# Kernel tuning notes

Hardware: AMD Instinct MI355X
Metric: run time of the kernel (lower is better)

The kernel has to match this reference:

```python
import jax, jax.numpy as jnp
import numpy as np

IN, OUT, RANK, ALPHA, GS = 4096, 4096, 16, 32, 64
SCALING = ALPHA / RANK  # alpha / rank = 2.0


def setup_inputs() -> dict:
    key = jax.random.key(0)
    k1, k2, k3, k4, k5 = jax.random.split(key, 5)
    x = jax.random.normal(k1, (4, 2048, IN), dtype=jnp.float32)
    # signed int4 codes in [-8, 7]
    q_w = jax.random.randint(k2, (OUT, IN), -8, 8, dtype=jnp.int32)
    # per-group absmax scales (positive, small)
    scales = jax.random.uniform(k3, (OUT, IN // GS), dtype=jnp.float32) * 0.02 + 1e-3
    lora_A = jax.random.normal(k4, (RANK, IN), dtype=jnp.float32) * 0.02
    lora_B = jax.random.normal(k5, (OUT, RANK), dtype=jnp.float32) * 0.02
    return {"x": x, "q_w": q_w, "scales": scales, "lora_A": lora_A, "lora_B": lora_B}


def reference(x, q_w, scales, lora_A, lora_B):
    # Dequantize 4-bit base weight: blockwise symmetric, group_size=GS along in_features.
    # W[o, g*GS + j] = q[o, g*GS + j] * scales[o, g]
    W = (q_w.astype(jnp.float32).reshape(OUT, IN // GS, GS)
         * scales[:, :, None]).reshape(OUT, IN)
    # Frozen base layer: y = x @ W^T (Linear4bit, no bias)
    base_output = jnp.einsum('bsi,oi->bso', x, W)
    # LoRA branch (dropout p=0 -> identity): B(A(x)) * (alpha/rank)
    lora_output = jnp.einsum('bsr,or->bso', jnp.einsum('bsi,ri->bsr', x, lora_A), lora_B) * SCALING
    return base_output + lora_output
```

## Files before the change

kernel.cpp:

```cpp
#include <hip/hip_runtime.h>
#include <hip/hip_bf16.h>


typedef unsigned short u16;
typedef __attribute__((ext_vector_type(8))) short bf16x8;
typedef __attribute__((ext_vector_type(4))) float f32x4;
typedef __attribute__((ext_vector_type(4))) int i32x4;

#define M_DIM 8192
#define N_DIM 4096
#define K_DIM 4096
#define BK 64
#define KT_MAIN 64
#define NT 65

__device__ static inline u16 f2bf(float f) {
    union { float f; unsigned u; } v; v.f = f;
    unsigned r = v.u + 0x7fffu + ((v.u >> 16) & 1u);
    return (u16)(r >> 16);
}

__device__ static inline void gload16(const void* g, void* s) {
    __builtin_amdgcn_global_load_lds(
        (const __attribute__((address_space(1))) void*)g,
        (__attribute__((address_space(3))) void*)s, 16, 0, 0);
}

__global__ __launch_bounds__(256) void wprep_kernel(
        const int* __restrict__ q, const float* __restrict__ scales,
        u16* __restrict__ Wb) {
    int idx = blockIdx.x * 256 + threadIdx.x;
    int o  = idx >> 9;
    int kc = (idx & 511) << 3;
    float s = scales[(o << 6) + (kc >> 6)];
    const i32x4* qp = (const i32x4*)(q + (size_t)o * K_DIM + kc);
    i32x4 q0 = __builtin_nontemporal_load(qp);
    i32x4 q1 = __builtin_nontemporal_load(qp + 1);
    ushort4 r0, r1;
    r0.x = f2bf((float)q0.x * s); r0.y = f2bf((float)q0.y * s);
    r0.z = f2bf((float)q0.z * s); r0.w = f2bf((float)q0.w * s);
    r1.x = f2bf((float)q1.x * s); r1.y = f2bf((float)q1.y * s);
    r1.z = f2bf((float)q1.z * s); r1.w = f2bf((float)q1.w * s);
    *(ushort4*)&Wb[(size_t)o * K_DIM + kc]     = r0;
    *(ushort4*)&Wb[(size_t)o * K_DIM + kc + 4] = r1;
}

__global__ __launch_bounds__(256) void bprep_kernel(
        const float* __restrict__ lora_B, u16* __restrict__ B2) {
    int idx = blockIdx.x * 256 + threadIdx.x;
    int o = idx >> 6, r = idx & 63;
    B2[idx] = (r < 16) ? f2bf(lora_B[o * 16 + r]) : (u16)0;
}

__global__ __launch_bounds__(256) void xprep_kernel(
        const float* __restrict__ x, const float* __restrict__ lora_A,
        u16* __restrict__ xb, u16* __restrict__ t2) {
    const int tid = threadIdx.x, w = tid >> 6, l = tid & 63;
    const int rb = blockIdx.x * 8 + w * 2;
    float acc[2][16];
#pragma unroll
    for (int j = 0; j < 2; ++j)
#pragma unroll
        for (int r = 0; r < 16; ++r) acc[j][r] = 0.f;

    for (int i = 0; i < 16; ++i) {
        int k0 = i * 256 + l * 4;
        f32x4 x0 = __builtin_nontemporal_load(
                        (const f32x4*)&x[(size_t)rb * K_DIM + k0]);
        f32x4 x1 = __builtin_nontemporal_load(
                        (const f32x4*)&x[(size_t)(rb + 1) * K_DIM + k0]);
        ushort4 o0, o1;
        o0.x = f2bf(x0.x); o0.y = f2bf(x0.y); o0.z = f2bf(x0.z); o0.w = f2bf(x0.w);
        o1.x = f2bf(x1.x); o1.y = f2bf(x1.y); o1.z = f2bf(x1.z); o1.w = f2bf(x1.w);
        *(ushort4*)&xb[(size_t)rb * K_DIM + k0]       = o0;
        *(ushort4*)&xb[(size_t)(rb + 1) * K_DIM + k0] = o1;
#pragma unroll
        for (int r = 0; r < 16; ++r) {
            f32x4 av = *(const f32x4*)&lora_A[(size_t)r * K_DIM + k0];
            acc[0][r] += x0.x * av.x + x0.y * av.y + x0.z * av.z + x0.w * av.w;
            acc[1][r] += x1.x * av.x + x1.y * av.y + x1.z * av.z + x1.w * av.w;
        }
    }
#pragma unroll
    for (int j = 0; j < 2; ++j)
#pragma unroll
        for (int r = 0; r < 16; ++r) {
            float v = acc[j][r];
            v += __shfl_xor(v, 32); v += __shfl_xor(v, 16);
            v += __shfl_xor(v, 8);  v += __shfl_xor(v, 4);
            v += __shfl_xor(v, 2);  v += __shfl_xor(v, 1);
            acc[j][r] = v;
        }
    float lo = 0.f, hi = 0.f;
#pragma unroll
    for (int j = 0; j < 2; ++j)
#pragma unroll
        for (int c = 0; c < 8; ++c)
            if (l == j * 32 + c) { lo = acc[j][2 * c]; hi = acc[j][2 * c + 1]; }
    unsigned pack = (unsigned)f2bf(2.0f * lo) | ((unsigned)f2bf(2.0f * hi) << 16);
    *(unsigned*)&t2[(size_t)(rb + (l >> 5)) * 64 + (l & 31) * 2] = pack;
}

__global__ __launch_bounds__(512, 2) void qlora_gemm(
        const u16* __restrict__ xb, const u16* __restrict__ Wb,
        const u16* __restrict__ t2, const u16* __restrict__ B2,
        float* __restrict__ out) {
    __shared__ u16 lds[2][32768];
    int bid = blockIdx.x;
    int x8 = bid & 7, sq = bid >> 3;
    int bm = (x8 & 1) * 16 + (sq & 15);
    int bn = (x8 >> 1) * 4 + (sq >> 4);
    const int tid = threadIdx.x, w = tid >> 6, l = tid & 63;
    const int wr = w >> 2, wc = w & 3;
    const int fr = l & 15, fq = l >> 4;
    const int s0 = fq ^ (fr & 7);

    const int sw16 = ((l & 7) ^ ((l >> 3) & 7)) << 4;
    const int rl   = w * 8 + (l >> 3);
    const int rA0  = bm * 256 + rl;
    const int rB0  = bn * 256 + rl;
    char* ldsC = (char*)&lds[0][0];
    const int dst = w * 1024 + l * 16;

    const int arow = (wr * 128 + fr) * 128;
    const int brow = 32768 + (wc * 64 + fr) * 128;

    f32x4 acc[8][4] = {};

    auto stage = [&](int kt, int buf) {
        char* base = ldsC + buf * 65536;
        if (kt < KT_MAIN) {
            size_t ko = (size_t)kt * 128;
#pragma unroll
            for (int o = 0; o < 4; ++o) {
                gload16((const char*)xb + ((size_t)(rA0 + o * 64) * 8192 + sw16) + ko,
                        base + dst + o * 8192);
                gload16((const char*)Wb + ((size_t)(rB0 + o * 64) * 8192 + sw16) + ko,
                        base + 32768 + dst + o * 8192);
            }
        } else {
#pragma unroll
            for (int o = 0; o < 4; ++o) {
                gload16((const char*)t2 + ((size_t)(rA0 + o * 64) * 128 + sw16),
                        base + dst + o * 8192);
                gload16((const char*)B2 + ((size_t)(rB0 + o * 64) * 128 + sw16),
                        base + 32768 + dst + o * 8192);
            }
        }
    };

    stage(0, 0);
    asm volatile("s_waitcnt vmcnt(0)" ::: "memory");
    __builtin_amdgcn_s_barrier();
    asm volatile("" ::: "memory");

    bf16x8 a0[8], b0[4], a1[8], b1[4];
#pragma unroll
    for (int j = 0; j < 4; ++j)
        b0[j] = *(const bf16x8*)(ldsC + brow + j * 2048 + s0 * 16);
#pragma unroll
    for (int i = 0; i < 8; ++i)
        a0[i] = *(const bf16x8*)(ldsC + arow + i * 2048 + s0 * 16);

    for (int t = 0; t < NT; ++t) {
        const char* cb = ldsC + (t & 1) * 65536;

#pragma unroll
        for (int j = 0; j < 4; ++j)
            b1[j] = *(const bf16x8*)(cb + brow + j * 2048 + (s0 ^ 4) * 16);
#pragma unroll
        for (int i = 0; i < 8; ++i)
            a1[i] = *(const bf16x8*)(cb + arow + i * 2048 + (s0 ^ 4) * 16);
        if (t + 1 < NT) stage(t + 1, (t + 1) & 1);
        __builtin_amdgcn_sched_barrier(0);

        __builtin_amdgcn_s_setprio(1);
#pragma unroll
        for (int i = 0; i < 8; ++i)
#pragma unroll
            for (int j = 0; j < 4; ++j)
                acc[i][j] = __builtin_amdgcn_mfma_f32_16x16x32_bf16(
                                a0[i], b0[j], acc[i][j], 0, 0, 0);
        __builtin_amdgcn_s_setprio(0);
        __builtin_amdgcn_sched_barrier(0);

        asm volatile("s_waitcnt lgkmcnt(0)" ::: "memory");
        asm volatile("s_waitcnt vmcnt(0)" ::: "memory");
        __builtin_amdgcn_s_barrier();
        asm volatile("" ::: "memory");

        if (t + 1 < NT) {
            const char* nb = ldsC + ((t + 1) & 1) * 65536;
#pragma unroll
            for (int j = 0; j < 4; ++j)
                b0[j] = *(const bf16x8*)(nb + brow + j * 2048 + s0 * 16);
#pragma unroll
            for (int i = 0; i < 8; ++i)
                a0[i] = *(const bf16x8*)(nb + arow + i * 2048 + s0 * 16);
        }
        __builtin_amdgcn_sched_barrier(0);

        __builtin_amdgcn_s_setprio(1);
#pragma unroll
        for (int i = 0; i < 8; ++i)
#pragma unroll
            for (int j = 0; j < 4; ++j)
                acc[i][j] = __builtin_amdgcn_mfma_f32_16x16x32_bf16(
                                a1[i], b1[j], acc[i][j], 0, 0, 0);
        __builtin_amdgcn_s_setprio(0);
        __builtin_amdgcn_sched_barrier(0);
    }

    float* obase = out + (size_t)(bm * 256 + wr * 128 + fq * 4) * N_DIM
                       + bn * 256 + wc * 64 + fr;
#pragma unroll
    for (int i = 0; i < 8; ++i)
#pragma unroll
        for (int j = 0; j < 4; ++j)
#pragma unroll
            for (int r = 0; r < 4; ++r)
                obase[(size_t)(i * 16 + r) * N_DIM + j * 16] = acc[i][j][r];
}

extern "C" void kernel_launch(void* const* d_in, const int* in_sizes, int n_in,
                              void* d_out, int out_size, void* d_ws, size_t ws_size,
                              hipStream_t stream) {
    const float* x      = (const float*)d_in[0];
    const int*   qw     = (const int*)d_in[1];
    const float* scales = (const float*)d_in[2];
    const float* lora_A = (const float*)d_in[3];
    const float* lora_B = (const float*)d_in[4];
    float* out = (float*)d_out;

    char* ws = (char*)d_ws;
    u16* xb = (u16*)(ws);
    u16* Wb = (u16*)(ws + 67108864);
    u16* t2 = (u16*)(ws + 100663296);
    u16* B2 = (u16*)(ws + 101711872);

    wprep_kernel<<<8192, 256, 0, stream>>>(qw, scales, Wb);
    bprep_kernel<<<1024, 256, 0, stream>>>(lora_B, B2);
    xprep_kernel<<<1024, 256, 0, stream>>>(x, lora_A, xb, t2);
    qlora_gemm<<<dim3(512), 512, 0, stream>>>(xb, Wb, t2, B2, out);
}
```

Before: 314.1 us.

## Merge prep kernels into one launch and deepen GEMM prefetch pipeline

Folds the three preprocessing kernels (weight dequant, LoRA-B pad, x conversion plus LoRA-A projection) into one kernel dispatched by block index. This removes two launches and lets the three jobs run concurrently on the GPU. The GEMM main loop is restructured to issue the global-to-LDS stage for the next tile at the top of each iteration, with a two-stage prologue. LDS fragment reads are interleaved with the MFMA half-steps so reads of one half overlap compute on the other, at the cost of more complex waitcnt ordering in the double-buffered LDS.

```diff
diff --git a/kernel.cpp b/kernel.cpp
--- a/kernel.cpp
+++ b/kernel.cpp
@@ -26,79 +26,79 @@
         (__attribute__((address_space(3))) void*)s, 16, 0, 0);
 }
 
-__global__ __launch_bounds__(256) void wprep_kernel(
+__global__ __launch_bounds__(256) void prep_kernel(
         const int* __restrict__ q, const float* __restrict__ scales,
-        u16* __restrict__ Wb) {
-    int idx = blockIdx.x * 256 + threadIdx.x;
-    int o  = idx >> 9;
-    int kc = (idx & 511) << 3;
-    float s = scales[(o << 6) + (kc >> 6)];
-    const i32x4* qp = (const i32x4*)(q + (size_t)o * K_DIM + kc);
-    i32x4 q0 = __builtin_nontemporal_load(qp);
-    i32x4 q1 = __builtin_nontemporal_load(qp + 1);
-    ushort4 r0, r1;
-    r0.x = f2bf((float)q0.x * s); r0.y = f2bf((float)q0.y * s);
-    r0.z = f2bf((float)q0.z * s); r0.w = f2bf((float)q0.w * s);
-    r1.x = f2bf((float)q1.x * s); r1.y = f2bf((float)q1.y * s);
-    r1.z = f2bf((float)q1.z * s); r1.w = f2bf((float)q1.w * s);
-    *(ushort4*)&Wb[(size_t)o * K_DIM + kc]     = r0;
-    *(ushort4*)&Wb[(size_t)o * K_DIM + kc + 4] = r1;
-}
-
-__global__ __launch_bounds__(256) void bprep_kernel(
-        const float* __restrict__ lora_B, u16* __restrict__ B2) {
-    int idx = blockIdx.x * 256 + threadIdx.x;
-    int o = idx >> 6, r = idx & 63;
-    B2[idx] = (r < 16) ? f2bf(lora_B[o * 16 + r]) : (u16)0;
-}
-
-__global__ __launch_bounds__(256) void xprep_kernel(
-        const float* __restrict__ x, const float* __restrict__ lora_A,
+        const float* __restrict__ lora_B, const float* __restrict__ x,
+        const float* __restrict__ lora_A,
+        u16* __restrict__ Wb, u16* __restrict__ B2,
         u16* __restrict__ xb, u16* __restrict__ t2) {
-    const int tid = threadIdx.x, w = tid >> 6, l = tid & 63;
-    const int rb = blockIdx.x * 8 + w * 2;
-    float acc[2][16];
-#pragma unroll
-    for (int j = 0; j < 2; ++j)
-#pragma unroll
-        for (int r = 0; r < 16; ++r) acc[j][r] = 0.f;
-
-    for (int i = 0; i < 16; ++i) {
-        int k0 = i * 256 + l * 4;
-        f32x4 x0 = __builtin_nontemporal_load(
-                        (const f32x4*)&x[(size_t)rb * K_DIM + k0]);
-        f32x4 x1 = __builtin_nontemporal_load(
-                        (const f32x4*)&x[(size_t)(rb + 1) * K_DIM + k0]);
-        ushort4 o0, o1;
-        o0.x = f2bf(x0.x); o0.y = f2bf(x0.y); o0.z = f2bf(x0.z); o0.w = f2bf(x0.w);
-        o1.x = f2bf(x1.x); o1.y = f2bf(x1.y); o1.z = f2bf(x1.z); o1.w = f2bf(x1.w);
-        *(ushort4*)&xb[(size_t)rb * K_DIM + k0]       = o0;
-        *(ushort4*)&xb[(size_t)(rb + 1) * K_DIM + k0] = o1;
-#pragma unroll
-        for (int r = 0; r < 16; ++r) {
-            f32x4 av = *(const f32x4*)&lora_A[(size_t)r * K_DIM + k0];
-            acc[0][r] += x0.x * av.x + x0.y * av.y + x0.z * av.z + x0.w * av.w;
-            acc[1][r] += x1.x * av.x + x1.y * av.y + x1.z * av.z + x1.w * av.w;
+    const int tid = threadIdx.x;
+    int b = blockIdx.x;
+    if (b < 1024) {
+        const int w = tid >> 6, l = tid & 63;
+        const int rb = b * 8 + w * 2;
+        float acc[2][16];
+#pragma unroll
+        for (int j = 0; j < 2; ++j)
+#pragma unroll
+            for (int r = 0; r < 16; ++r) acc[j][r] = 0.f;
+
+        for (int i = 0; i < 16; ++i) {
+            int k0 = i * 256 + l * 4;
+            f32x4 x0 = __builtin_nontemporal_load(
+                            (const f32x4*)&x[(size_t)rb * K_DIM + k0]);
+            f32x4 x1 = __builtin_nontemporal_load(
+                            (const f32x4*)&x[(size_t)(rb + 1) * K_DIM + k0]);
+            ushort4 o0, o1;
+            o0.x = f2bf(x0.x); o0.y = f2bf(x0.y); o0.z = f2bf(x0.z); o0.w = f2bf(x0.w);
+            o1.x = f2bf(x1.x); o1.y = f2bf(x1.y); o1.z = f2bf(x1.z); o1.w = f2bf(x1.w);
+            *(ushort4*)&xb[(size_t)rb * K_DIM + k0]       = o0;
+            *(ushort4*)&xb[(size_t)(rb + 1) * K_DIM + k0] = o1;
+#pragma unroll
+            for (int r = 0; r < 16; ++r) {
+                f32x4 av = *(const f32x4*)&lora_A[(size_t)r * K_DIM + k0];
+                acc[0][r] += x0.x * av.x + x0.y * av.y + x0.z * av.z + x0.w * av.w;
+                acc[1][r] += x1.x * av.x + x1.y * av.y + x1.z * av.z + x1.w * av.w;
+            }
         }
+#pragma unroll
+        for (int j = 0; j < 2; ++j)
+#pragma unroll
+            for (int r = 0; r < 16; ++r) {
+                float v = acc[j][r];
+                v += __shfl_xor(v, 32); v += __shfl_xor(v, 16);
+                v += __shfl_xor(v, 8);  v += __shfl_xor(v, 4);
+                v += __shfl_xor(v, 2);  v += __shfl_xor(v, 1);
+                acc[j][r] = v;
+            }
+        float lo = 0.f, hi = 0.f;
+#pragma unroll
+        for (int j = 0; j < 2; ++j)
+#pragma unroll
+            for (int c = 0; c < 8; ++c)
+                if (l == j * 32 + c) { lo = acc[j][2 * c]; hi = acc[j][2 * c + 1]; }
+        unsigned pack = (unsigned)f2bf(2.0f * lo) | ((unsigned)f2bf(2.0f * hi) << 16);
+        *(unsigned*)&t2[(size_t)(rb + (l >> 5)) * 64 + (l & 31) * 2] = pack;
+    } else if (b < 9216) {
+        int idx = (b - 1024) * 256 + tid;
+        int o  = idx >> 9;
+        int kc = (idx & 511) << 3;
+        float s = scales[(o << 6) + (kc >> 6)];
+        const i32x4* qp = (const i32x4*)(q + (size_t)o * K_DIM + kc);
+        i32x4 q0 = __builtin_nontemporal_load(qp);
+        i32x4 q1 = __builtin_nontemporal_load(qp + 1);
+        ushort4 r0, r1;
+        r0.x = f2bf((float)q0.x * s); r0.y = f2bf((float)q0.y * s);
+        r0.z = f2bf((float)q0.z * s); r0.w = f2bf((float)q0.w * s);
+        r1.x = f2bf((float)q1.x * s); r1.y = f2bf((float)q1.y * s);
+        r1.z = f2bf((float)q1.z * s); r1.w = f2bf((float)q1.w * s);
+        *(ushort4*)&Wb[(size_t)o * K_DIM + kc]     = r0;
+        *(ushort4*)&Wb[(size_t)o * K_DIM + kc + 4] = r1;
+    } else {
+        int idx = (b - 9216) * 256 + tid;
+        int o = idx >> 6, r = idx & 63;
+        B2[idx] = (r < 16) ? f2bf(lora_B[o * 16 + r]) : (u16)0;
     }
-#pragma unroll
-    for (int j = 0; j < 2; ++j)
-#pragma unroll
-        for (int r = 0; r < 16; ++r) {
-            float v = acc[j][r];
-            v += __shfl_xor(v, 32); v += __shfl_xor(v, 16);
-            v += __shfl_xor(v, 8);  v += __shfl_xor(v, 4);
-            v += __shfl_xor(v, 2);  v += __shfl_xor(v, 1);
-            acc[j][r] = v;
-        }
-    float lo = 0.f, hi = 0.f;
-#pragma unroll
-    for (int j = 0; j < 2; ++j)
-#pragma unroll
-        for (int c = 0; c < 8; ++c)
-            if (l == j * 32 + c) { lo = acc[j][2 * c]; hi = acc[j][2 * c + 1]; }
-    unsigned pack = (unsigned)f2bf(2.0f * lo) | ((unsigned)f2bf(2.0f * hi) << 16);
-    *(unsigned*)&t2[(size_t)(rb + (l >> 5)) * 64 + (l & 31) * 2] = pack;
 }
 
 __global__ __launch_bounds__(512, 2) void qlora_gemm(
@@ -126,6 +126,7 @@
     const int brow = 32768 + (wc * 64 + fr) * 128;
 
     f32x4 acc[8][4] = {};
+    bf16x8 a0[8], b0[4], a1[8], b1[4];
 
     auto stage = [&](int kt, int buf) {
         char* base = ldsC + buf * 65536;
@@ -149,31 +150,23 @@
         }
     };
 
-    stage(0, 0);
-    asm volatile("s_waitcnt vmcnt(0)" ::: "memory");
-    __builtin_amdgcn_s_barrier();
-    asm volatile("" ::: "memory");
-
-    bf16x8 a0[8], b0[4], a1[8], b1[4];
-#pragma unroll
-    for (int j = 0; j < 4; ++j)
-        b0[j] = *(const bf16x8*)(ldsC + brow + j * 2048 + s0 * 16);
-#pragma unroll
-    for (int i = 0; i < 8; ++i)
-        a0[i] = *(const bf16x8*)(ldsC + arow + i * 2048 + s0 * 16);
-
-    for (int t = 0; t < NT; ++t) {
-        const char* cb = ldsC + (t & 1) * 65536;
-
+    auto read0 = [&](const char* cb) {
+#pragma unroll
+        for (int j = 0; j < 4; ++j)
+            b0[j] = *(const bf16x8*)(cb + brow + j * 2048 + s0 * 16);
+#pragma unroll
+        for (int i = 0; i < 8; ++i)
+            a0[i] = *(const bf16x8*)(cb + arow + i * 2048 + s0 * 16);
+    };
+    auto read1 = [&](const char* cb) {
 #pragma unroll
         for (int j = 0; j < 4; ++j)
             b1[j] = *(const bf16x8*)(cb + brow + j * 2048 + (s0 ^ 4) * 16);
 #pragma unroll
         for (int i = 0; i < 8; ++i)
             a1[i] = *(const bf16x8*)(cb + arow + i * 2048 + (s0 ^ 4) * 16);
-        if (t + 1 < NT) stage(t + 1, (t + 1) & 1);
-        __builtin_amdgcn_sched_barrier(0);
-
+    };
+    auto mfma0 = [&]() {
         __builtin_amdgcn_s_setprio(1);
 #pragma unroll
         for (int i = 0; i < 8; ++i)
@@ -182,34 +175,54 @@
                 acc[i][j] = __builtin_amdgcn_mfma_f32_16x16x32_bf16(
                                 a0[i], b0[j], acc[i][j], 0, 0, 0);
         __builtin_amdgcn_s_setprio(0);
-        __builtin_amdgcn_sched_barrier(0);
-
+    };
+    auto mfma1 = [&]() {
+        __builtin_amdgcn_s_setprio(1);
+#pragma unroll
+        for (int i = 0; i < 8; ++i)
+#pragma unroll
+            for (int j = 0; j < 4; ++j)
+                acc[i][j] = __builtin_amdgcn_mfma_f32_16x16x32_bf16(
+                                a1[i], b1[j], acc[i][j], 0, 0, 0);
+        __builtin_amdgcn_s_setprio(0);
+    };
+
+    stage(0, 0);
+    stage(1, 1);
+    asm volatile("s_waitcnt vmcnt(8)" ::: "memory");
+    __builtin_amdgcn_s_barrier();
+    asm volatile("" ::: "memory");
+
+    read0(ldsC);
+    asm volatile("s_waitcnt lgkmcnt(0)" ::: "memory");
+    __builtin_amdgcn_sched_barrier(0);
+    read1(ldsC);
+    __builtin_amdgcn_sched_barrier(0);
+    mfma0();
+    __builtin_amdgcn_sched_barrier(0);
+    asm volatile("s_waitcnt lgkmcnt(0)" ::: "memory");
+    asm volatile("s_waitcnt vmcnt(0)" ::: "memory");
+    __builtin_amdgcn_s_barrier();
+    asm volatile("" ::: "memory");
+
+    for (int t = 1; t < NT; ++t) {
+        const char* cb = ldsC + (t & 1) * 65536;
+        if (t + 1 < NT) stage(t + 1, (t + 1) & 1);
+        read0(cb);
+        __builtin_amdgcn_sched_barrier(0);
+        mfma1();
+        __builtin_amdgcn_sched_barrier(0);
+        asm volatile("s_waitcnt lgkmcnt(0)" ::: "memory");
+        read1(cb);
+        __builtin_amdgcn_sched_barrier(0);
+        mfma0();
+        __builtin_amdgcn_sched_barrier(0);
         asm volatile("s_waitcnt lgkmcnt(0)" ::: "memory");
         asm volatile("s_waitcnt vmcnt(0)" ::: "memory");
         __builtin_amdgcn_s_barrier();
         asm volatile("" ::: "memory");
-
-        if (t + 1 < NT) {
-            const char* nb = ldsC + ((t + 1) & 1) * 65536;
-#pragma unroll
-            for (int j = 0; j < 4; ++j)
-                b0[j] = *(const bf16x8*)(nb + brow + j * 2048 + s0 * 16);
-#pragma unroll
-            for (int i = 0; i < 8; ++i)
-                a0[i] = *(const bf16x8*)(nb + arow + i * 2048 + s0 * 16);
-        }
-        __builtin_amdgcn_sched_barrier(0);
-
-        __builtin_amdgcn_s_setprio(1);
-#pragma unroll
-        for (int i = 0; i < 8; ++i)
-#pragma unroll
-            for (int j = 0; j < 4; ++j)
-                acc[i][j] = __builtin_amdgcn_mfma_f32_16x16x32_bf16(
-                                a1[i], b1[j], acc[i][j], 0, 0, 0);
-        __builtin_amdgcn_s_setprio(0);
-        __builtin_amdgcn_sched_barrier(0);
     }
+    mfma1();
 
     float* obase = out + (size_t)(bm * 256 + wr * 128 + fq * 4) * N_DIM
                        + bn * 256 + wc * 64 + fr;
@@ -238,8 +251,7 @@
     u16* t2 = (u16*)(ws + 100663296);
     u16* B2 = (u16*)(ws + 101711872);
 
-    wprep_kernel<<<8192, 256, 0, stream>>>(qw, scales, Wb);
-    bprep_kernel<<<1024, 256, 0, stream>>>(lora_B, B2);
-    xprep_kernel<<<1024, 256, 0, stream>>>(x, lora_A, xb, t2);
+    prep_kernel<<<10240, 256, 0, stream>>>(qw, scales, lora_B, x, lora_A,
+                                           Wb, B2, xb, t2);
     qlora_gemm<<<dim3(512), 512, 0, stream>>>(xb, Wb, t2, B2, out);
 }
```

Result: slower. 320.8 us (+2.1%).
